# Kernel tuning notes

Hardware: AMD Instinct MI355X
Metric: run time of the kernel (lower is better)

The kernel has to match this reference:

```python
import jax, jax.numpy as jnp
import numpy as np

N = 20000
F_IN = 128
HID = 128
HEADS = 8
NCLS = 18
NEG_SLOPE = 0.2


def setup_inputs() -> dict:
    key = jax.random.key(0)
    ks = jax.random.split(key, 12)
    x = jax.random.normal(ks[0], (N, F_IN), dtype=jnp.float32)
    edge_index = jax.random.randint(ks[1], (2, 200000), 0, N)
    sc1 = 1.0 / np.sqrt(F_IN)
    sc2 = 1.0 / np.sqrt(HEADS * HID)
    W1 = jax.random.normal(ks[2], (F_IN, HEADS * HID), dtype=jnp.float32) * sc1
    a1_src = jax.random.normal(ks[3], (HEADS, HID), dtype=jnp.float32) * sc1
    a1_dst = jax.random.normal(ks[4], (HEADS, HID), dtype=jnp.float32) * sc1
    b1 = jnp.zeros((HEADS * HID,), dtype=jnp.float32)
    W2 = jax.random.normal(ks[5], (HEADS * HID, NCLS), dtype=jnp.float32) * sc2
    a2_src = jax.random.normal(ks[6], (1, NCLS), dtype=jnp.float32) * sc2
    a2_dst = jax.random.normal(ks[7], (1, NCLS), dtype=jnp.float32) * sc2
    b2 = jnp.zeros((NCLS,), dtype=jnp.float32)
    return {"x": x, "edge_index": edge_index, "W1": W1, "a1_src": a1_src,
            "a1_dst": a1_dst, "b1": b1, "W2": W2, "a2_src": a2_src,
            "a2_dst": a2_dst, "b2": b2}


def gat_conv(x, src, dst, W, a_src, a_dst, b, heads, out_ch):
    n = x.shape[0]
    h = (x @ W).reshape(n, heads, out_ch)              # [N,H,C]
    alpha_s = jnp.sum(h * a_src, axis=-1)              # [N,H]
    alpha_d = jnp.sum(h * a_dst, axis=-1)              # [N,H]
    e = jax.nn.leaky_relu(alpha_s[src] + alpha_d[dst], NEG_SLOPE)  # [E,H]
    # per-destination softmax (segment softmax)
    m = jax.ops.segment_max(e, dst, num_segments=n)
    e = jnp.exp(e - m[dst])
    z = jax.ops.segment_sum(e, dst, num_segments=n)
    alpha = e / (z[dst] + 1e-16)                       # [E,H]
    out = jax.ops.segment_sum(alpha[:, :, None] * h[src], dst, num_segments=n)
    return out.reshape(n, heads * out_ch) + b


def reference(x, edge_index, W1, a1_src, a1_dst, b1, W2, a2_src, a2_dst, b2):
    n = x.shape[0]
    # PyG GATConv adds self-loops by default
    loops = jnp.arange(n, dtype=edge_index.dtype)
    src = jnp.concatenate([edge_index[0], loops])
    dst = jnp.concatenate([edge_index[1], loops])
    h = gat_conv(x, src, dst, W1, a1_src, a1_dst, b1, HEADS, HID)
    h = jax.nn.relu(h)
    # F.dropout(training=self.training) is identity in eval mode
    out = gat_conv(h, src, dst, W2, a2_src, a2_dst, b2, 1, NCLS)
    return out
```

## Files before the change

kernel.cpp:

```cpp
#include <hip/hip_runtime.h>
#include <math.h>

#define FIN 128
#define NH 8
#define HC 128
#define HD (NH*HC)
#define NC 18
#define NEG 0.2f

typedef __attribute__((ext_vector_type(8))) short bf16x8;
typedef __attribute__((ext_vector_type(4))) float f32x4;

__device__ __forceinline__ float lrelu(float v){ return v > 0.f ? v : NEG*v; }

__device__ __forceinline__ unsigned short f2b(float f){
  unsigned u = __float_as_uint(f);
  unsigned r = (u + 0x7fffu + ((u >> 16) & 1u)) >> 16;
  return (unsigned short)r;
}
__device__ __forceinline__ float b2f_lo(unsigned u){ return __uint_as_float(u << 16); }
__device__ __forceinline__ float b2f_hi(unsigned u){ return __uint_as_float(u & 0xffff0000u); }

__global__ void hist_k(const int* __restrict__ ei, int E0, int N, int* __restrict__ deg){
  int e = blockIdx.x*256 + threadIdx.x;
  int tot = E0 + N;
  if (e >= tot) return;
  int dst = (e < E0) ? ei[E0 + e] : (e - E0);
  atomicAdd(&deg[dst], 1);
}

__global__ __launch_bounds__(1024) void scan_k(const int* __restrict__ deg, int N,
                                               int* __restrict__ off, int* __restrict__ cursor){
  __shared__ int wsum[16];
  __shared__ int s_carry;
  int t = threadIdx.x, lane = t & 63, wid = t >> 6;
  if (t == 0) s_carry = 0;
  __syncthreads();
  for (int base = 0; base < N; base += 1024) {
    int i = base + t;
    int v = (i < N) ? deg[i] : 0;
    int x = v;
    #pragma unroll
    for (int o = 1; o < 64; o <<= 1) {
      int y = __shfl_up(x, o, 64);
      if (lane >= o) x += y;
    }
    if (lane == 63) wsum[wid] = x;
    __syncthreads();
    if (wid == 0) {
      int wv = (lane < 16) ? wsum[lane] : 0;
      #pragma unroll
      for (int o = 1; o < 16; o <<= 1) {
        int y = __shfl_up(wv, o, 64);
        if (lane >= o) wv += y;
      }
      if (lane < 16) wsum[lane] = wv;
    }
    __syncthreads();
    int woff = (wid > 0) ? wsum[wid-1] : 0;
    int carry = s_carry;
    int exc = x - v + woff + carry;
    if (i < N) { off[i] = exc; cursor[i] = exc; }
    __syncthreads();
    if (t == 1023) s_carry = carry + wsum[15];
    __syncthreads();
  }
  if (t == 0) off[N] = s_carry;
}

__global__ void scatter_k(const int* __restrict__ ei, int E0, int N,
                          int* __restrict__ cursor, int* __restrict__ csr){
  int e = blockIdx.x*256 + threadIdx.x;
  int tot = E0 + N;
  if (e >= tot) return;
  int src, dst;
  if (e < E0) { src = ei[e]; dst = ei[E0 + e]; }
  else        { src = e - E0; dst = src; }
  int p = atomicAdd(&cursor[dst], 1);
  csr[p] = src;
}

__global__ __launch_bounds__(256) void xcvt_k(const float* __restrict__ x,
                                              unsigned short* __restrict__ xb, int total8){
  int i = blockIdx.x*256 + threadIdx.x;
  if (i >= total8) return;
  const float4* p = (const float4*)x + (size_t)i*2;
  float4 a = p[0], b = p[1];
  uint4 o;
  o.x = (unsigned)f2b(a.x) | ((unsigned)f2b(a.y) << 16);
  o.y = (unsigned)f2b(a.z) | ((unsigned)f2b(a.w) << 16);
  o.z = (unsigned)f2b(b.x) | ((unsigned)f2b(b.y) << 16);
  o.w = (unsigned)f2b(b.z) | ((unsigned)f2b(b.w) << 16);
  ((uint4*)xb)[i] = o;
}

__global__ __launch_bounds__(256) void w1t_k(const float* __restrict__ W1,
                                             unsigned short* __restrict__ w1t){
  __shared__ unsigned short sT[FIN][64+2];
  int t = threadIdx.x;
  int n0 = blockIdx.x * 64;
  #pragma unroll
  for (int i = 0; i < 32; ++i) {
    int idx = i*256 + t;
    int k = idx >> 6, nl = idx & 63;
    sT[k][nl] = f2b(W1[(size_t)k*HD + n0 + nl]);
  }
  __syncthreads();
  #pragma unroll
  for (int i = 0; i < 16; ++i) {
    int nl = i*4 + (t >> 6);
    int kp = t & 63;
    unsigned u = (unsigned)sT[2*kp][nl] | ((unsigned)sT[2*kp+1][nl] << 16);
    *(unsigned*)&w1t[(size_t)(n0+nl)*FIN + 2*kp] = u;
  }
}

__global__ __launch_bounds__(256) void gemm1_mfma_k(const unsigned short* __restrict__ xb,
                                                    const unsigned short* __restrict__ w1t,
                                                    unsigned short* __restrict__ g1b, int N){
  __shared__ unsigned short sA[128][136];
  __shared__ unsigned short sB[128][136];
  int t = threadIdx.x, lane = t & 63, wid = t >> 6;
  int bm = blockIdx.x * 128;
  int bn = blockIdx.y * 128;
  #pragma unroll
  for (int i = 0; i < 2; ++i) {
    int idx = i*256 + t;
    int row = idx >> 2, seg = idx & 3;
    int gm = bm + row;
    uint4 a0,a1,a2,a3;
    if (gm < N) {
      const uint4* gp = (const uint4*)(xb + (size_t)gm*FIN + seg*32);
      a0 = gp[0]; a1 = gp[1]; a2 = gp[2]; a3 = gp[3];
    } else {
      a0 = a1 = a2 = a3 = make_uint4(0,0,0,0);
    }
    uint4* lp = (uint4*)&sA[row][seg*32];
    lp[0]=a0; lp[1]=a1; lp[2]=a2; lp[3]=a3;
  }
  #pragma unroll
  for (int i = 0; i < 2; ++i) {
    int idx = i*256 + t;
    int row = idx >> 2, seg = idx & 3;
    const uint4* gp = (const uint4*)(w1t + (size_t)(bn + row)*FIN + seg*32);
    uint4* lp = (uint4*)&sB[row][seg*32];
    lp[0]=gp[0]; lp[1]=gp[1]; lp[2]=gp[2]; lp[3]=gp[3];
  }
  __syncthreads();
  int wr = wid >> 1, wc = wid & 1;
  int lr = lane & 15, kb = lane >> 4;
  f32x4 acc[4][4];
  #pragma unroll
  for (int mi = 0; mi < 4; ++mi)
    #pragma unroll
    for (int ni = 0; ni < 4; ++ni) {
      f32x4 z = {0.f, 0.f, 0.f, 0.f};
      acc[mi][ni] = z;
    }
  #pragma unroll
  for (int ks = 0; ks < 4; ++ks) {
    int ko = ks*32 + kb*8;
    bf16x8 a[4], b[4];
    #pragma unroll
    for (int mi = 0; mi < 4; ++mi)
      a[mi] = *(const bf16x8*)&sA[wr*64 + mi*16 + lr][ko];
    #pragma unroll
    for (int ni = 0; ni < 4; ++ni)
      b[ni] = *(const bf16x8*)&sB[wc*64 + ni*16 + lr][ko];
    #pragma unroll
    for (int mi = 0; mi < 4; ++mi)
      #pragma unroll
      for (int ni = 0; ni < 4; ++ni)
        acc[mi][ni] = __builtin_amdgcn_mfma_f32_16x16x32_bf16(a[mi], b[ni], acc[mi][ni], 0, 0, 0);
  }
  #pragma unroll
  for (int mi = 0; mi < 4; ++mi)
    #pragma unroll
    for (int ni = 0; ni < 4; ++ni) {
      int col = bn + wc*64 + ni*16 + lr;
      #pragma unroll
      for (int r = 0; r < 4; ++r) {
        int row = bm + wr*64 + mi*16 + kb*4 + r;
        if (row < N) g1b[(size_t)row*HD + col] = f2b(acc[mi][ni][r]);
      }
    }
}

__global__ __launch_bounds__(256) void alpha1_k(const unsigned short* __restrict__ g1b,
    const float* __restrict__ a1s, const float* __restrict__ a1d,
    float* __restrict__ as1, float* __restrict__ ad1, int N){
  int n = blockIdx.x, t = threadIdx.x;
  int h = t >> 5;
  int cc = (t & 31) << 2;
  uint2 raw = *(const uint2*)(g1b + (size_t)n*HD + (t << 2));
  float h0 = b2f_lo(raw.x), h1 = b2f_hi(raw.x), h2 = b2f_lo(raw.y), h3 = b2f_hi(raw.y);
  float4 av = *(const float4*)&a1s[h*HC + cc];
  float4 bv = *(const float4*)&a1d[h*HC + cc];
  float s = h0*av.x + h1*av.y + h2*av.z + h3*av.w;
  float d = h0*bv.x + h1*bv.y + h2*bv.z + h3*bv.w;
  #pragma unroll
  for (int o = 16; o > 0; o >>= 1) {
    s += __shfl_xor(s, o, 32);
    d += __shfl_xor(d, o, 32);
  }
  if ((t & 31) == 0) { as1[n*NH + h] = s; ad1[n*NH + h] = d; }
}

__global__ __launch_bounds__(256) void attn1_k(const unsigned short* __restrict__ g1b,
    const float* __restrict__ as1, const float* __restrict__ ad1,
    const int* __restrict__ off, const int* __restrict__ csr,
    const float* __restrict__ b1, unsigned short* __restrict__ hb, int N){
  int t = threadIdx.x, lane = t & 63, wid = t >> 6;
  int d = blockIdx.x*4 + wid;
  if (d >= N) return;
  int beg = off[d], end = off[d+1], deg = end - beg;

  int hr = lane & 7;
  float adr = ad1[d*NH + hr];
  float m = -1e30f, z = 0.f;
  for (int j = lane >> 3; j < deg; j += 8) {
    int s = csr[beg + j];
    float e = lrelu(as1[s*NH + hr] + adr);
    if (e > m) { z = z*__expf(m - e) + 1.f; m = e; }
    else       { z += __expf(e - m); }
  }
  #pragma unroll
  for (int o = 8; o < 64; o <<= 1) {
    float mo = __shfl_xor(m, o, 64), zo = __shfl_xor(z, o, 64);
    float mn = fmaxf(m, mo);
    z = z*__expf(m - mn) + zo*__expf(mo - mn);
    m = mn;
  }
  int hg = lane >> 3;
  float mg   = __shfl(m,   hg, 64);
  float zg   = __shfl(z,   hg, 64);
  float adg  = __shfl(adr, hg, 64);
  float zinv = 1.f / (zg + 1e-16f);

  float acc[16];
  #pragma unroll
  for (int i = 0; i < 16; ++i) acc[i] = 0.f;
  for (int j = 0; j < deg; ++j) {
    int s = csr[beg + j];
    float e = lrelu(as1[s*NH + hg] + adg);
    float w = __expf(e - mg) * zinv;
    const uint4* p = (const uint4*)(g1b + (size_t)s*HD) + lane*2;
    uint4 r0 = p[0], r1 = p[1];
    acc[ 0] += w*b2f_lo(r0.x); acc[ 1] += w*b2f_hi(r0.x);
    acc[ 2] += w*b2f_lo(r0.y); acc[ 3] += w*b2f_hi(r0.y);
    acc[ 4] += w*b2f_lo(r0.z); acc[ 5] += w*b2f_hi(r0.z);
    acc[ 6] += w*b2f_lo(r0.w); acc[ 7] += w*b2f_hi(r0.w);
    acc[ 8] += w*b2f_lo(r1.x); acc[ 9] += w*b2f_hi(r1.x);
    acc[10] += w*b2f_lo(r1.y); acc[11] += w*b2f_hi(r1.y);
    acc[12] += w*b2f_lo(r1.z); acc[13] += w*b2f_hi(r1.z);
    acc[14] += w*b2f_lo(r1.w); acc[15] += w*b2f_hi(r1.w);
  }
  int cb = lane*16;
  uint o[8];
  #pragma unroll
  for (int q = 0; q < 4; ++q) {
    float4 bv = *(const float4*)&b1[cb + q*4];
    float v0 = fmaxf(acc[q*4+0] + bv.x, 0.f);
    float v1 = fmaxf(acc[q*4+1] + bv.y, 0.f);
    float v2 = fmaxf(acc[q*4+2] + bv.z, 0.f);
    float v3 = fmaxf(acc[q*4+3] + bv.w, 0.f);
    o[q*2+0] = (unsigned)f2b(v0) | ((unsigned)f2b(v1) << 16);
    o[q*2+1] = (unsigned)f2b(v2) | ((unsigned)f2b(v3) << 16);
  }
  uint4* dst = (uint4*)(hb + (size_t)d*HD) + lane*2;
  dst[0] = make_uint4(o[0], o[1], o[2], o[3]);
  dst[1] = make_uint4(o[4], o[5], o[6], o[7]);
}

__global__ __launch_bounds__(256) void gemm2_k(const unsigned short* __restrict__ hb,
    const float* __restrict__ W2, const float* __restrict__ a2s_g, const float* __restrict__ a2d_g,
    float* __restrict__ g2, float* __restrict__ as2, float* __restrict__ ad2, int N){
  __shared__ unsigned short sW[HD*NC];
  __shared__ float red[4][64][NC+1];
  int t = threadIdx.x, lane = t & 63, wid = t >> 6;
  int n0 = blockIdx.x * 64;
  #pragma unroll
  for (int i = 0; i < (HD*NC)/256; ++i) {
    int idx = i*256 + t;
    sW[idx] = f2b(W2[idx]);
  }
  __syncthreads();
  int n = n0 + lane;
  bool valid = (n < N);
  float acc[NC];
  #pragma unroll
  for (int c = 0; c < NC; ++c) acc[c] = 0.f;
  int k0beg = wid * 256;
  for (int k0 = k0beg; k0 < k0beg + 256; k0 += 8) {
    uint4 raw = valid ? *(const uint4*)(hb + (size_t)n*HD + k0) : make_uint4(0,0,0,0);
    float a[8];
    a[0]=b2f_lo(raw.x); a[1]=b2f_hi(raw.x); a[2]=b2f_lo(raw.y); a[3]=b2f_hi(raw.y);
    a[4]=b2f_lo(raw.z); a[5]=b2f_hi(raw.z); a[6]=b2f_lo(raw.w); a[7]=b2f_hi(raw.w);
    #pragma unroll
    for (int kk = 0; kk < 8; ++kk) {
      const unsigned* wr = (const unsigned*)(sW + (size_t)(k0 + kk)*NC);
      float av = a[kk];
      #pragma unroll
      for (int c2 = 0; c2 < NC/2; ++c2) {
        unsigned u = wr[c2];
        acc[2*c2+0] += av * b2f_lo(u);
        acc[2*c2+1] += av * b2f_hi(u);
      }
    }
  }
  #pragma unroll
  for (int c = 0; c < NC; ++c) red[wid][lane][c] = acc[c];
  __syncthreads();
  if (wid == 0 && valid) {
    float tot[NC];
    #pragma unroll
    for (int c = 0; c < NC; ++c)
      tot[c] = red[0][lane][c] + red[1][lane][c] + red[2][lane][c] + red[3][lane][c];
    float s = 0.f, dd = 0.f;
    #pragma unroll
    for (int c = 0; c < NC; ++c) {
      s  += tot[c]*a2s_g[c];
      dd += tot[c]*a2d_g[c];
      g2[(size_t)n*NC + c] = tot[c];
    }
    as2[n] = s; ad2[n] = dd;
  }
}

__global__ __launch_bounds__(256) void attn2_k(const float* __restrict__ g2,
    const float* __restrict__ as2, const float* __restrict__ ad2,
    const int* __restrict__ off, const int* __restrict__ csr,
    const float* __restrict__ b2, float* __restrict__ out, int N){
  int t = threadIdx.x, lane = t & 63, wid = t >> 6;
  int d = blockIdx.x*4 + wid;
  if (d >= N) return;
  int beg = off[d], end = off[d+1];
  float adv = ad2[d];
  float lm = -1e30f;
  for (int j = beg + lane; j < end; j += 64)
    lm = fmaxf(lm, lrelu(as2[csr[j]] + adv));
  #pragma unroll
  for (int o = 32; o > 0; o >>= 1) lm = fmaxf(lm, __shfl_xor(lm, o, 64));
  float lz = 0.f;
  for (int j = beg + lane; j < end; j += 64)
    lz += __expf(lrelu(as2[csr[j]] + adv) - lm);
  #pragma unroll
  for (int o = 32; o > 0; o >>= 1) lz += __shfl_xor(lz, o, 64);
  float zinv = 1.f / (lz + 1e-16f);
  if (lane < NC) {
    float acc = 0.f;
    for (int j = beg; j < end; ++j) {
      int s = csr[j];
      float w = __expf(lrelu(as2[s] + adv) - lm) * zinv;
      acc += w * g2[(size_t)s*NC + lane];
    }
    out[(size_t)d*NC + lane] = acc + b2[lane];
  }
}

extern "C" void kernel_launch(void* const* d_in, const int* in_sizes, int n_in,
                              void* d_out, int out_size, void* d_ws, size_t ws_size,
                              hipStream_t stream){
  const float* x   = (const float*)d_in[0];
  const int*   ei  = (const int*)d_in[1];
  const float* W1  = (const float*)d_in[2];
  const float* a1s = (const float*)d_in[3];
  const float* a1d = (const float*)d_in[4];
  const float* b1  = (const float*)d_in[5];
  const float* W2  = (const float*)d_in[6];
  const float* a2s = (const float*)d_in[7];
  const float* a2d = (const float*)d_in[8];
  const float* b2  = (const float*)d_in[9];
  float* out = (float*)d_out;
  int N  = in_sizes[0] / FIN;
  int E0 = in_sizes[1] / 2;
  int Etot = E0 + N;

  float* as1 = (float*)d_ws;
  float* ad1 = as1 + (size_t)N*NH;
  float* g2  = ad1 + (size_t)N*NH;
  float* as2 = g2 + (size_t)N*NC;
  float* ad2 = as2 + N;
  unsigned short* g1b = (unsigned short*)(ad2 + N);
  unsigned short* hb  = g1b + (size_t)N*HD;
  int* deg    = (int*)(hb + (size_t)N*HD);
  int* off    = deg + N;
  int* cursor = off + N + 4;
  int* csr    = cursor + N;
  unsigned short* xb  = hb;
  unsigned short* w1t = hb + (size_t)N*FIN;

  hipMemsetAsync(deg, 0, sizeof(int)*(size_t)N, stream);
  hist_k<<<(Etot+255)/256, 256, 0, stream>>>(ei, E0, N, deg);
  scan_k<<<1, 1024, 0, stream>>>(deg, N, off, cursor);
  scatter_k<<<(Etot+255)/256, 256, 0, stream>>>(ei, E0, N, cursor, csr);

  int total8 = N*FIN/8;
  xcvt_k<<<(total8+255)/256, 256, 0, stream>>>(x, xb, total8);
  w1t_k<<<HD/64, 256, 0, stream>>>(W1, w1t);

  dim3 g1grid((N+127)/128, HD/128);
  gemm1_mfma_k<<<g1grid, 256, 0, stream>>>(xb, w1t, g1b, N);
  alpha1_k<<<N, 256, 0, stream>>>(g1b, a1s, a1d, as1, ad1, N);
  attn1_k<<<(N+3)/4, 256, 0, stream>>>(g1b, as1, ad1, off, csr, b1, hb, N);
  gemm2_k<<<(N+63)/64, 256, 0, stream>>>(hb, W2, a2s, a2d, g2, as2, ad2, N);
  attn2_k<<<(N+3)/4, 256, 0, stream>>>(g2, as2, ad2, off, csr, b2, out, N);
}
```

Measured before the change: 289.6 us.

## Use single-pass online softmax in attention kernels, pre-convert W2, and batch alpha1 per wave

attn1 and attn2 drop the separate max/sum pass and use a single-pass online softmax with rescaling. attn1 is unrolled by 4 edges to keep more gathers in flight, and attn2 spreads edges over three lane groups of 18 instead of leaving most lanes idle. W2 is converted to padded bf16 once by a new kernel, so each gemm2 block no longer converts it into shared memory; gemm2 now reads it from global/cache with vector loads. alpha1 processes one node per wave instead of one per 256-thread block, and the extra rescale multiplies on each new maximum add some cost.

```diff
diff --git a/kernel.cpp b/kernel.cpp
--- a/kernel.cpp
+++ b/kernel.cpp
@@ -6,6 +6,7 @@
 #define HC 128
 #define HD (NH*HC)
 #define NC 18
+#define NCP 24
 #define NEG 0.2f
 
 typedef __attribute__((ext_vector_type(8))) short bf16x8;
@@ -20,6 +21,13 @@
 }
 __device__ __forceinline__ float b2f_lo(unsigned u){ return __uint_as_float(u << 16); }
 __device__ __forceinline__ float b2f_hi(unsigned u){ return __uint_as_float(u & 0xffff0000u); }
+
+__device__ __forceinline__ void acc8(float* a, float w, uint4 r){
+  a[0] += w*b2f_lo(r.x); a[1] += w*b2f_hi(r.x);
+  a[2] += w*b2f_lo(r.y); a[3] += w*b2f_hi(r.y);
+  a[4] += w*b2f_lo(r.z); a[5] += w*b2f_hi(r.z);
+  a[6] += w*b2f_lo(r.w); a[7] += w*b2f_hi(r.w);
+}
 
 __global__ void hist_k(const int* __restrict__ ei, int E0, int N, int* __restrict__ deg){
   int e = blockIdx.x*256 + threadIdx.x;
@@ -115,6 +123,14 @@
   }
 }
 
+__global__ __launch_bounds__(256) void w2cvt_k(const float* __restrict__ W2,
+                                               unsigned short* __restrict__ w2b){
+  int idx = blockIdx.x*256 + threadIdx.x;
+  if (idx >= HD*NC) return;
+  int k = idx / NC, c = idx - k*NC;
+  w2b[k*NCP + c] = f2b(W2[idx]);
+}
+
 __global__ __launch_bounds__(256) void gemm1_mfma_k(const unsigned short* __restrict__ xb,
                                                     const unsigned short* __restrict__ w1t,
                                                     unsigned short* __restrict__ g1b, int N){
@@ -189,21 +205,32 @@
 __global__ __launch_bounds__(256) void alpha1_k(const unsigned short* __restrict__ g1b,
     const float* __restrict__ a1s, const float* __restrict__ a1d,
     float* __restrict__ as1, float* __restrict__ ad1, int N){
-  int n = blockIdx.x, t = threadIdx.x;
-  int h = t >> 5;
-  int cc = (t & 31) << 2;
-  uint2 raw = *(const uint2*)(g1b + (size_t)n*HD + (t << 2));
-  float h0 = b2f_lo(raw.x), h1 = b2f_hi(raw.x), h2 = b2f_lo(raw.y), h3 = b2f_hi(raw.y);
-  float4 av = *(const float4*)&a1s[h*HC + cc];
-  float4 bv = *(const float4*)&a1d[h*HC + cc];
-  float s = h0*av.x + h1*av.y + h2*av.z + h3*av.w;
-  float d = h0*bv.x + h1*bv.y + h2*bv.z + h3*bv.w;
-  #pragma unroll
-  for (int o = 16; o > 0; o >>= 1) {
-    s += __shfl_xor(s, o, 32);
-    d += __shfl_xor(d, o, 32);
-  }
-  if ((t & 31) == 0) { as1[n*NH + h] = s; ad1[n*NH + h] = d; }
+  int t = threadIdx.x, lane = t & 63, wid = t >> 6;
+  int n = blockIdx.x*4 + wid;
+  if (n >= N) return;
+  int c0 = lane * 16;
+  int h = lane >> 3;
+  const uint4* p = (const uint4*)(g1b + (size_t)n*HD) + lane*2;
+  uint4 r0 = p[0], r1 = p[1];
+  float hv[16];
+  hv[0]=b2f_lo(r0.x); hv[1]=b2f_hi(r0.x); hv[2]=b2f_lo(r0.y); hv[3]=b2f_hi(r0.y);
+  hv[4]=b2f_lo(r0.z); hv[5]=b2f_hi(r0.z); hv[6]=b2f_lo(r0.w); hv[7]=b2f_hi(r0.w);
+  hv[8]=b2f_lo(r1.x); hv[9]=b2f_hi(r1.x); hv[10]=b2f_lo(r1.y); hv[11]=b2f_hi(r1.y);
+  hv[12]=b2f_lo(r1.z); hv[13]=b2f_hi(r1.z); hv[14]=b2f_lo(r1.w); hv[15]=b2f_hi(r1.w);
+  float s = 0.f, dd = 0.f;
+  #pragma unroll
+  for (int q = 0; q < 4; ++q) {
+    float4 av = *(const float4*)&a1s[c0 + q*4];
+    float4 bv = *(const float4*)&a1d[c0 + q*4];
+    s  += hv[q*4+0]*av.x + hv[q*4+1]*av.y + hv[q*4+2]*av.z + hv[q*4+3]*av.w;
+    dd += hv[q*4+0]*bv.x + hv[q*4+1]*bv.y + hv[q*4+2]*bv.z + hv[q*4+3]*bv.w;
+  }
+  #pragma unroll
+  for (int o = 1; o < 8; o <<= 1) {
+    s  += __shfl_xor(s, o, 8);
+    dd += __shfl_xor(dd, o, 8);
+  }
+  if ((lane & 7) == 0) { as1[n*NH + h] = s; ad1[n*NH + h] = dd; }
 }
 
 __global__ __launch_bounds__(256) void attn1_k(const unsigned short* __restrict__ g1b,
@@ -213,57 +240,72 @@
   int t = threadIdx.x, lane = t & 63, wid = t >> 6;
   int d = blockIdx.x*4 + wid;
   if (d >= N) return;
-  int beg = off[d], end = off[d+1], deg = end - beg;
-
-  int hr = lane & 7;
-  float adr = ad1[d*NH + hr];
+  int beg = off[d], deg = off[d+1] - beg;
+  int hg = lane >> 3;
+  float adg = ad1[d*NH + hg];
   float m = -1e30f, z = 0.f;
-  for (int j = lane >> 3; j < deg; j += 8) {
-    int s = csr[beg + j];
-    float e = lrelu(as1[s*NH + hr] + adr);
-    if (e > m) { z = z*__expf(m - e) + 1.f; m = e; }
-    else       { z += __expf(e - m); }
-  }
-  #pragma unroll
-  for (int o = 8; o < 64; o <<= 1) {
-    float mo = __shfl_xor(m, o, 64), zo = __shfl_xor(z, o, 64);
-    float mn = fmaxf(m, mo);
-    z = z*__expf(m - mn) + zo*__expf(mo - mn);
-    m = mn;
-  }
-  int hg = lane >> 3;
-  float mg   = __shfl(m,   hg, 64);
-  float zg   = __shfl(z,   hg, 64);
-  float adg  = __shfl(adr, hg, 64);
-  float zinv = 1.f / (zg + 1e-16f);
-
   float acc[16];
   #pragma unroll
   for (int i = 0; i < 16; ++i) acc[i] = 0.f;
-  for (int j = 0; j < deg; ++j) {
-    int s = csr[beg + j];
-    float e = lrelu(as1[s*NH + hg] + adg);
-    float w = __expf(e - mg) * zinv;
+
+  int j = 0;
+  for (; j + 4 <= deg; j += 4) {
+    int s0 = csr[beg+j+0], s1 = csr[beg+j+1], s2 = csr[beg+j+2], s3 = csr[beg+j+3];
+    const uint4* p0 = (const uint4*)(g1b + (size_t)s0*HD) + lane*2;
+    const uint4* p1 = (const uint4*)(g1b + (size_t)s1*HD) + lane*2;
+    const uint4* p2 = (const uint4*)(g1b + (size_t)s2*HD) + lane*2;
+    const uint4* p3 = (const uint4*)(g1b + (size_t)s3*HD) + lane*2;
+    uint4 r00 = p0[0], r01 = p0[1];
+    uint4 r10 = p1[0], r11 = p1[1];
+    uint4 r20 = p2[0], r21 = p2[1];
+    uint4 r30 = p3[0], r31 = p3[1];
+    float e0 = lrelu(as1[s0*NH+hg] + adg);
+    float e1 = lrelu(as1[s1*NH+hg] + adg);
+    float e2 = lrelu(as1[s2*NH+hg] + adg);
+    float e3 = lrelu(as1[s3*NH+hg] + adg);
+    float em = fmaxf(fmaxf(e0,e1), fmaxf(e2,e3));
+    if (em > m) {
+      float sc = __expf(m - em);
+      z *= sc;
+      #pragma unroll
+      for (int i = 0; i < 16; ++i) acc[i] *= sc;
+      m = em;
+    }
+    float w0 = __expf(e0 - m), w1 = __expf(e1 - m);
+    float w2 = __expf(e2 - m), w3 = __expf(e3 - m);
+    z += w0 + w1 + w2 + w3;
+    acc8(acc, w0, r00); acc8(acc+8, w0, r01);
+    acc8(acc, w1, r10); acc8(acc+8, w1, r11);
+    acc8(acc, w2, r20); acc8(acc+8, w2, r21);
+    acc8(acc, w3, r30); acc8(acc+8, w3, r31);
+  }
+  for (; j < deg; ++j) {
+    int s = csr[beg+j];
     const uint4* p = (const uint4*)(g1b + (size_t)s*HD) + lane*2;
     uint4 r0 = p[0], r1 = p[1];
-    acc[ 0] += w*b2f_lo(r0.x); acc[ 1] += w*b2f_hi(r0.x);
-    acc[ 2] += w*b2f_lo(r0.y); acc[ 3] += w*b2f_hi(r0.y);
-    acc[ 4] += w*b2f_lo(r0.z); acc[ 5] += w*b2f_hi(r0.z);
-    acc[ 6] += w*b2f_lo(r0.w); acc[ 7] += w*b2f_hi(r0.w);
-    acc[ 8] += w*b2f_lo(r1.x); acc[ 9] += w*b2f_hi(r1.x);
-    acc[10] += w*b2f_lo(r1.y); acc[11] += w*b2f_hi(r1.y);
-    acc[12] += w*b2f_lo(r1.z); acc[13] += w*b2f_hi(r1.z);
-    acc[14] += w*b2f_lo(r1.w); acc[15] += w*b2f_hi(r1.w);
-  }
+    float e = lrelu(as1[s*NH+hg] + adg);
+    if (e > m) {
+      float sc = __expf(m - e);
+      z *= sc;
+      #pragma unroll
+      for (int i = 0; i < 16; ++i) acc[i] *= sc;
+      m = e;
+    }
+    float w = __expf(e - m);
+    z += w;
+    acc8(acc, w, r0); acc8(acc+8, w, r1);
+  }
+
+  float zinv = 1.f / (z + 1e-16f);
   int cb = lane*16;
   uint o[8];
   #pragma unroll
   for (int q = 0; q < 4; ++q) {
     float4 bv = *(const float4*)&b1[cb + q*4];
-    float v0 = fmaxf(acc[q*4+0] + bv.x, 0.f);
-    float v1 = fmaxf(acc[q*4+1] + bv.y, 0.f);
-    float v2 = fmaxf(acc[q*4+2] + bv.z, 0.f);
-    float v3 = fmaxf(acc[q*4+3] + bv.w, 0.f);
+    float v0 = fmaxf(acc[q*4+0]*zinv + bv.x, 0.f);
+    float v1 = fmaxf(acc[q*4+1]*zinv + bv.y, 0.f);
+    float v2 = fmaxf(acc[q*4+2]*zinv + bv.z, 0.f);
+    float v3 = fmaxf(acc[q*4+3]*zinv + bv.w, 0.f);
     o[q*2+0] = (unsigned)f2b(v0) | ((unsigned)f2b(v1) << 16);
     o[q*2+1] = (unsigned)f2b(v2) | ((unsigned)f2b(v3) << 16);
   }
@@ -273,18 +315,11 @@
 }
 
 __global__ __launch_bounds__(256) void gemm2_k(const unsigned short* __restrict__ hb,
-    const float* __restrict__ W2, const float* __restrict__ a2s_g, const float* __restrict__ a2d_g,
+    const unsigned short* __restrict__ w2b, const float* __restrict__ a2s_g, const float* __restrict__ a2d_g,
     float* __restrict__ g2, float* __restrict__ as2, float* __restrict__ ad2, int N){
-  __shared__ unsigned short sW[HD*NC];
-  __shared__ float red[4][64][NC+1];
+  __shared__ float red[3][64][NC+1];
   int t = threadIdx.x, lane = t & 63, wid = t >> 6;
   int n0 = blockIdx.x * 64;
-  #pragma unroll
-  for (int i = 0; i < (HD*NC)/256; ++i) {
-    int idx = i*256 + t;
-    sW[idx] = f2b(W2[idx]);
-  }
-  __syncthreads();
   int n = n0 + lane;
   bool valid = (n < N);
   float acc[NC];
@@ -298,24 +333,32 @@
     a[4]=b2f_lo(raw.z); a[5]=b2f_hi(raw.z); a[6]=b2f_lo(raw.w); a[7]=b2f_hi(raw.w);
     #pragma unroll
     for (int kk = 0; kk < 8; ++kk) {
-      const unsigned* wr = (const unsigned*)(sW + (size_t)(k0 + kk)*NC);
+      const unsigned* wr = (const unsigned*)(w2b + (size_t)(k0 + kk)*NCP);
+      uint4 u0 = *(const uint4*)(wr);
+      uint4 u1 = *(const uint4*)(wr + 4);
+      unsigned u2 = wr[8];
       float av = a[kk];
-      #pragma unroll
-      for (int c2 = 0; c2 < NC/2; ++c2) {
-        unsigned u = wr[c2];
-        acc[2*c2+0] += av * b2f_lo(u);
-        acc[2*c2+1] += av * b2f_hi(u);
-      }
-    }
-  }
-  #pragma unroll
-  for (int c = 0; c < NC; ++c) red[wid][lane][c] = acc[c];
+      acc[0]  += av * b2f_lo(u0.x); acc[1]  += av * b2f_hi(u0.x);
+      acc[2]  += av * b2f_lo(u0.y); acc[3]  += av * b2f_hi(u0.y);
+      acc[4]  += av * b2f_lo(u0.z); acc[5]  += av * b2f_hi(u0.z);
+      acc[6]  += av * b2f_lo(u0.w); acc[7]  += av * b2f_hi(u0.w);
+      acc[8]  += av * b2f_lo(u1.x); acc[9]  += av * b2f_hi(u1.x);
+      acc[10] += av * b2f_lo(u1.y); acc[11] += av * b2f_hi(u1.y);
+      acc[12] += av * b2f_lo(u1.z); acc[13] += av * b2f_hi(u1.z);
+      acc[14] += av * b2f_lo(u1.w); acc[15] += av * b2f_hi(u1.w);
+      acc[16] += av * b2f_lo(u2);   acc[17] += av * b2f_hi(u2);
+    }
+  }
+  if (wid > 0) {
+    #pragma unroll
+    for (int c = 0; c < NC; ++c) red[wid-1][lane][c] = acc[c];
+  }
   __syncthreads();
   if (wid == 0 && valid) {
     float tot[NC];
     #pragma unroll
     for (int c = 0; c < NC; ++c)
-      tot[c] = red[0][lane][c] + red[1][lane][c] + red[2][lane][c] + red[3][lane][c];
+      tot[c] = acc[c] + red[0][lane][c] + red[1][lane][c] + red[2][lane][c];
     float s = 0.f, dd = 0.f;
     #pragma unroll
     for (int c = 0; c < NC; ++c) {
@@ -334,27 +377,45 @@
   int t = threadIdx.x, lane = t & 63, wid = t >> 6;
   int d = blockIdx.x*4 + wid;
   if (d >= N) return;
-  int beg = off[d], end = off[d+1];
+  int beg = off[d], deg = off[d+1] - beg;
   float adv = ad2[d];
-  float lm = -1e30f;
-  for (int j = beg + lane; j < end; j += 64)
-    lm = fmaxf(lm, lrelu(as2[csr[j]] + adv));
-  #pragma unroll
-  for (int o = 32; o > 0; o >>= 1) lm = fmaxf(lm, __shfl_xor(lm, o, 64));
-  float lz = 0.f;
-  for (int j = beg + lane; j < end; j += 64)
-    lz += __expf(lrelu(as2[csr[j]] + adv) - lm);
-  #pragma unroll
-  for (int o = 32; o > 0; o >>= 1) lz += __shfl_xor(lz, o, 64);
-  float zinv = 1.f / (lz + 1e-16f);
+  int g = lane / 18;
+  int c = lane - g*18;
+  float m = -1e30f, z = 0.f, acc = 0.f;
+  if (g < 3) {
+    int j = g;
+    for (; j + 3 < deg; j += 6) {
+      int sa = csr[beg+j], sb = csr[beg+j+3];
+      float va = g2[(size_t)sa*NC + c];
+      float vb = g2[(size_t)sb*NC + c];
+      float ea = lrelu(as2[sa] + adv);
+      float eb = lrelu(as2[sb] + adv);
+      float em = fmaxf(ea, eb);
+      if (em > m) { float sc = __expf(m - em); z *= sc; acc *= sc; m = em; }
+      float wa = __expf(ea - m), wb = __expf(eb - m);
+      z += wa + wb;
+      acc += wa*va + wb*vb;
+    }
+    for (; j < deg; j += 3) {
+      int s = csr[beg+j];
+      float v = g2[(size_t)s*NC + c];
+      float e = lrelu(as2[s] + adv);
+      if (e > m) { float sc = __expf(m - e); z *= sc; acc *= sc; m = e; }
+      float w = __expf(e - m);
+      z += w;
+      acc += w*v;
+    }
+  }
+  float m0 = __shfl(m, 0),  m1 = __shfl(m, 18), m2 = __shfl(m, 36);
+  float M  = fmaxf(m0, fmaxf(m1, m2));
+  float e0 = __expf(m0 - M), e1 = __expf(m1 - M), e2 = __expf(m2 - M);
+  float z0 = __shfl(z, 0),  z1 = __shfl(z, 18), z2 = __shfl(z, 36);
+  int cl = (lane < NC) ? lane : 0;
+  float a0 = __shfl(acc, cl), a1 = __shfl(acc, cl+18), a2 = __shfl(acc, cl+36);
   if (lane < NC) {
-    float acc = 0.f;
-    for (int j = beg; j < end; ++j) {
-      int s = csr[j];
-      float w = __expf(lrelu(as2[s] + adv) - lm) * zinv;
-      acc += w * g2[(size_t)s*NC + lane];
-    }
-    out[(size_t)d*NC + lane] = acc + b2[lane];
+    float Z = z0*e0 + z1*e1 + z2*e2;
+    float A = a0*e0 + a1*e1 + a2*e2;
+    out[(size_t)d*NC + lane] = A / (Z + 1e-16f) + b2[lane];
   }
 }
 
@@ -387,6 +448,7 @@
   int* off    = deg + N;
   int* cursor = off + N + 4;
   int* csr    = cursor + N;
+  unsigned short* w2b = (unsigned short*)(csr + Etot);
   unsigned short* xb  = hb;
   unsigned short* w1t = hb + (size_t)N*FIN;
 
@@ -398,11 +460,12 @@
   int total8 = N*FIN/8;
   xcvt_k<<<(total8+255)/256, 256, 0, stream>>>(x, xb, total8);
   w1t_k<<<HD/64, 256, 0, stream>>>(W1, w1t);
+  w2cvt_k<<<(HD*NC+255)/256, 256, 0, stream>>>(W2, w2b);
 
   dim3 g1grid((N+127)/128, HD/128);
   gemm1_mfma_k<<<g1grid, 256, 0, stream>>>(xb, w1t, g1b, N);
-  alpha1_k<<<N, 256, 0, stream>>>(g1b, a1s, a1d, as1, ad1, N);
+  alpha1_k<<<(N+3)/4, 256, 0, stream>>>(g1b, a1s, a1d, as1, ad1, N);
   attn1_k<<<(N+3)/4, 256, 0, stream>>>(g1b, as1, ad1, off, csr, b1, hb, N);
-  gemm2_k<<<(N+63)/64, 256, 0, stream>>>(hb, W2, a2s, a2d, g2, as2, ad2, N);
+  gemm2_k<<<(N+63)/64, 256, 0, stream>>>(hb, w2b, a2s, a2d, g2, as2, ad2, N);
   attn2_k<<<(N+3)/4, 256, 0, stream>>>(g2, as2, ad2, off, csr, b2, out, N);
 }
```

After: 293.4 us. No clear change (+1.3%).
